# Optimization experiments

Hardware: AMD Instinct MI355X
Metric: run time of the kernel (lower is better)

Reference implementation:

```python
import jax, jax.numpy as jnp
import numpy as np

N_NODES = 100000
HIDDEN = 128
N_EDGES = 640000


def setup_inputs() -> dict:
    key = jax.random.key(0)
    ks = jax.random.split(key, 7)
    x = jax.random.normal(ks[0], (N_NODES, HIDDEN), dtype=jnp.float32)
    # torch Linear weights, stored transposed for y = h @ W + b
    W1 = jax.random.normal(ks[1], (HIDDEN, HIDDEN), dtype=jnp.float32) * (1.0 / np.sqrt(HIDDEN))
    b1 = jax.random.normal(ks[2], (HIDDEN,), dtype=jnp.float32) * 0.01
    W2 = jax.random.normal(ks[3], (HIDDEN, 1), dtype=jnp.float32) * (1.0 / np.sqrt(HIDDEN))
    b2 = jax.random.normal(ks[4], (1,), dtype=jnp.float32) * 0.01
    edge_index = jax.random.randint(ks[5], (2, N_EDGES), 0, N_NODES, dtype=jnp.int64 if jax.config.jax_enable_x64 else jnp.int32)
    edge_index_neg = jax.random.randint(ks[6], (2, N_EDGES), 0, N_NODES, dtype=jnp.int64 if jax.config.jax_enable_x64 else jnp.int32)
    return {"x": x, "W1": W1, "b1": b1, "W2": W2, "b2": b2,
            "edge_index": edge_index, "edge_index_neg": edge_index_neg}


def _decode(x, W1, b1, W2, b2, ei):
    # gather endpoints and Hadamard product: [E, hidden]
    h = x[ei[0]] * x[ei[1]]
    # decoder = ReLU -> Linear(h,h) -> ReLU -> Linear(h,1); then sigmoid
    h = jax.nn.relu(h)
    h = jax.nn.relu(h @ W1 + b1)
    return jax.nn.sigmoid(h @ W2 + b2)  # [E, 1]


def reference(x, W1, b1, W2, b2, edge_index, edge_index_neg):
    edge_pos_pred = _decode(x, W1, b1, W2, b2, edge_index)
    edge_neg_pred = _decode(x, W1, b1, W2, b2, edge_index_neg)
    return jnp.concatenate([edge_pos_pred, edge_neg_pred], axis=0)  # [2E, 1]
```

## Files before the change

### kernel.cpp

```cpp
#include <hip/hip_runtime.h>
#include <hip/hip_bf16.h>

#define HID   128
#define PITCH 136
#define TPB   256

typedef __attribute__((ext_vector_type(8))) __bf16 bf16x8;
typedef __attribute__((ext_vector_type(4))) __bf16 bf16x4;
typedef __attribute__((ext_vector_type(4))) float  f32x4;

__global__ __launch_bounds__(TPB) void prep_kernel(
    const float* __restrict__ W1, __bf16* __restrict__ w1t,
    const float* __restrict__ x, __bf16* __restrict__ xb, int n_x4) {
  if (xb) {
    for (int i = blockIdx.x * TPB + threadIdx.x; i < n_x4; i += gridDim.x * TPB) {
      float4 a = reinterpret_cast<const float4*>(x)[i];
      bf16x4 v;
      v[0] = (__bf16)a.x; v[1] = (__bf16)a.y; v[2] = (__bf16)a.z; v[3] = (__bf16)a.w;
      reinterpret_cast<bf16x4*>(xb)[i] = v;
    }
  }
  if (blockIdx.x == 0 && w1t) {
    __shared__ float w[HID * HID];
    for (int i = threadIdx.x; i < HID * HID; i += TPB) w[i] = W1[i];
    __syncthreads();
    for (int c = threadIdx.x; c < HID * (HID / 8); c += TPB) {
      int n  = c >> 4;
      int k0 = (c & 15) << 3;
      bf16x8 v;
#pragma unroll
      for (int j = 0; j < 8; ++j) v[j] = (__bf16)w[(k0 + j) * HID + n];
      *reinterpret_cast<bf16x8*>(&w1t[n * PITCH + k0]) = v;
    }
  }
}

__global__ __launch_bounds__(TPB) void vgae_decode_kernel(
    const __bf16* __restrict__ xb,
    const __bf16* __restrict__ w1t,
    const float* __restrict__ b1,
    const float* __restrict__ W2,
    const float* __restrict__ b2,
    const int* __restrict__ eip,
    const int* __restrict__ ein,
    float* __restrict__ out,
    int E, int n_tiles)
{
  __shared__ __bf16 sW[HID * PITCH];
  __shared__ float  sb1[HID];
  __shared__ float  sw2[HID];

  {
    const uint4* srcp = reinterpret_cast<const uint4*>(w1t);
    uint4*       dstp = reinterpret_cast<uint4*>(sW);
    for (int i = threadIdx.x; i < (HID * PITCH) / 8; i += TPB) dstp[i] = srcp[i];
  }
  if (threadIdx.x < HID) {
    sb1[threadIdx.x] = b1[threadIdx.x];
    sw2[threadIdx.x] = W2[threadIdx.x];
  }
  __syncthreads();

  const int lane = threadIdx.x & 63;
  const int wave = threadIdx.x >> 6;
  const int m    = lane & 15;
  const int quad = lane >> 4;
  const float b2v = b2[0];

  int tile = blockIdx.x;
  int nsrc = 0, ndst = 0;
  if (tile < n_tiles) {
    const int e_base = tile * 64 + wave * 16;
    const int* ei = (e_base < E) ? eip : ein;
    const int  eo = (e_base < E) ? e_base : (e_base - E);
    nsrc = ei[eo + m];
    ndst = ei[E + eo + m];
  }

  for (; tile < n_tiles; tile += gridDim.x) {
    const int src = nsrc, dst = ndst;
    const __bf16* xs = xb + (size_t)src * HID;
    const __bf16* xd = xb + (size_t)dst * HID;

    bf16x8 S[4], D[4];
#pragma unroll
    for (int kt = 0; kt < 4; ++kt) {
      const int k0 = kt * 32 + quad * 8;
      S[kt] = *reinterpret_cast<const bf16x8*>(xs + k0);
      D[kt] = *reinterpret_cast<const bf16x8*>(xd + k0);
    }

    const int tn = tile + gridDim.x;
    if (tn < n_tiles) {
      const int e_base = tn * 64 + wave * 16;
      const int* ei = (e_base < E) ? eip : ein;
      const int  eo = (e_base < E) ? e_base : (e_base - E);
      nsrc = ei[eo + m];
      ndst = ei[E + eo + m];
    }

    f32x4 acc[8] = {};

#pragma unroll
    for (int kt = 0; kt < 4; ++kt) {
      const int k0 = kt * 32 + quad * 8;
      bf16x8 a;
#pragma unroll
      for (int j = 0; j < 8; ++j) {
        float p = (float)S[kt][j] * (float)D[kt][j];
        a[j] = (__bf16)fmaxf(p, 0.f);
      }
#pragma unroll
      for (int nt = 0; nt < 8; ++nt) {
        bf16x8 bfr = *reinterpret_cast<const bf16x8*>(&sW[(nt * 16 + m) * PITCH + k0]);
        acc[nt] = __builtin_amdgcn_mfma_f32_16x16x32_bf16(a, bfr, acc[nt], 0, 0, 0);
      }
    }

    float p[4] = {0.f, 0.f, 0.f, 0.f};
#pragma unroll
    for (int nt = 0; nt < 8; ++nt) {
      const int n = nt * 16 + m;
      const float b1n = sb1[n];
      const float w2n = sw2[n];
#pragma unroll
      for (int r = 0; r < 4; ++r) {
        float t = fmaxf(acc[nt][r] + b1n, 0.f);
        p[r] = fmaf(t, w2n, p[r]);
      }
    }
#pragma unroll
    for (int off = 1; off < 16; off <<= 1) {
#pragma unroll
      for (int r = 0; r < 4; ++r) p[r] += __shfl_xor(p[r], off, 64);
    }
    if (m == 0) {
      float4 o;
      o.x = 1.f / (1.f + __expf(-(p[0] + b2v)));
      o.y = 1.f / (1.f + __expf(-(p[1] + b2v)));
      o.z = 1.f / (1.f + __expf(-(p[2] + b2v)));
      o.w = 1.f / (1.f + __expf(-(p[3] + b2v)));
      *reinterpret_cast<float4*>(out + tile * 64 + wave * 16 + quad * 4) = o;
    }
  }
}

__global__ __launch_bounds__(TPB) void vgae_decode_fallback(
    const float* __restrict__ x,
    const float* __restrict__ W1,
    const float* __restrict__ b1,
    const float* __restrict__ W2,
    const float* __restrict__ b2,
    const int* __restrict__ eip,
    const int* __restrict__ ein,
    float* __restrict__ out,
    int E, int n_tiles)
{
  __shared__ __bf16 sW[HID * PITCH];
  __shared__ float  sb1[HID];
  __shared__ float  sw2[HID];
  for (int c = threadIdx.x; c < HID * (HID / 8); c += TPB) {
    int n = c >> 4, k0 = (c & 15) << 3;
    bf16x8 v;
#pragma unroll
    for (int j = 0; j < 8; ++j) v[j] = (__bf16)W1[(k0 + j) * HID + n];
    *reinterpret_cast<bf16x8*>(&sW[n * PITCH + k0]) = v;
  }
  if (threadIdx.x < HID) { sb1[threadIdx.x] = b1[threadIdx.x]; sw2[threadIdx.x] = W2[threadIdx.x]; }
  __syncthreads();
  const int lane = threadIdx.x & 63, wave = threadIdx.x >> 6;
  const int m = lane & 15, quad = lane >> 4;
  const float b2v = b2[0];
  for (int tile = blockIdx.x; tile < n_tiles; tile += gridDim.x) {
    const int e_base = tile * 64 + wave * 16;
    const int* ei = (e_base < E) ? eip : ein;
    const int  eo = (e_base < E) ? e_base : (e_base - E);
    const int src = ei[eo + m], dst = ei[E + eo + m];
    const float* xs = x + (size_t)src * HID;
    const float* xd = x + (size_t)dst * HID;
    f32x4 acc[8] = {};
#pragma unroll
    for (int kt = 0; kt < 4; ++kt) {
      const int k0 = kt * 32 + quad * 8;
      float4 s0 = *reinterpret_cast<const float4*>(xs + k0);
      float4 s1 = *reinterpret_cast<const float4*>(xs + k0 + 4);
      float4 d0 = *reinterpret_cast<const float4*>(xd + k0);
      float4 d1 = *reinterpret_cast<const float4*>(xd + k0 + 4);
      bf16x8 a;
      a[0] = (__bf16)fmaxf(s0.x * d0.x, 0.f); a[1] = (__bf16)fmaxf(s0.y * d0.y, 0.f);
      a[2] = (__bf16)fmaxf(s0.z * d0.z, 0.f); a[3] = (__bf16)fmaxf(s0.w * d0.w, 0.f);
      a[4] = (__bf16)fmaxf(s1.x * d1.x, 0.f); a[5] = (__bf16)fmaxf(s1.y * d1.y, 0.f);
      a[6] = (__bf16)fmaxf(s1.z * d1.z, 0.f); a[7] = (__bf16)fmaxf(s1.w * d1.w, 0.f);
#pragma unroll
      for (int nt = 0; nt < 8; ++nt) {
        bf16x8 bfr = *reinterpret_cast<const bf16x8*>(&sW[(nt * 16 + m) * PITCH + k0]);
        acc[nt] = __builtin_amdgcn_mfma_f32_16x16x32_bf16(a, bfr, acc[nt], 0, 0, 0);
      }
    }
    float p[4] = {0.f, 0.f, 0.f, 0.f};
#pragma unroll
    for (int nt = 0; nt < 8; ++nt) {
      const int n = nt * 16 + m;
      const float b1n = sb1[n], w2n = sw2[n];
#pragma unroll
      for (int r = 0; r < 4; ++r) p[r] = fmaf(fmaxf(acc[nt][r] + b1n, 0.f), w2n, p[r]);
    }
#pragma unroll
    for (int off = 1; off < 16; off <<= 1)
#pragma unroll
      for (int r = 0; r < 4; ++r) p[r] += __shfl_xor(p[r], off, 64);
    if (m == 0) {
      float4 o;
      o.x = 1.f / (1.f + __expf(-(p[0] + b2v)));
      o.y = 1.f / (1.f + __expf(-(p[1] + b2v)));
      o.z = 1.f / (1.f + __expf(-(p[2] + b2v)));
      o.w = 1.f / (1.f + __expf(-(p[3] + b2v)));
      *reinterpret_cast<float4*>(out + tile * 64 + wave * 16 + quad * 4) = o;
    }
  }
}

extern "C" void kernel_launch(void* const* d_in, const int* in_sizes, int n_in,
                              void* d_out, int out_size, void* d_ws, size_t ws_size,
                              hipStream_t stream) {
  const float* x  = (const float*)d_in[0];
  const float* W1 = (const float*)d_in[1];
  const float* b1 = (const float*)d_in[2];
  const float* W2 = (const float*)d_in[3];
  const float* b2 = (const float*)d_in[4];
  const int*  eip = (const int*)d_in[5];
  const int*  ein = (const int*)d_in[6];
  float* out = (float*)d_out;
  const int E = in_sizes[5] / 2;
  const int n_tiles = (2 * E) / 64;
  const int n_nodes = in_sizes[0] / HID;
  const int n_x4 = in_sizes[0] / 4;

  const size_t w1t_bytes = (size_t)HID * PITCH * sizeof(__bf16);
  const size_t xb_off    = 65536;
  const size_t xb_bytes  = (size_t)n_nodes * HID * sizeof(__bf16);

  __bf16* w1t = nullptr;
  __bf16* xb  = nullptr;
  if (ws_size >= w1t_bytes) w1t = (__bf16*)d_ws;
  if (ws_size >= xb_off + xb_bytes) xb = (__bf16*)((char*)d_ws + xb_off);

  if (w1t && xb) {
    int prep_grid = (n_x4 + TPB - 1) / TPB;
    if (prep_grid > 6400) prep_grid = 6400;
    prep_kernel<<<prep_grid, TPB, 0, stream>>>(W1, w1t, x, xb, n_x4);
    vgae_decode_kernel<<<2560, TPB, 0, stream>>>(xb, w1t, b1, W2, b2,
                                                 eip, ein, out, E, n_tiles);
  } else {
    vgae_decode_fallback<<<2560, TPB, 0, stream>>>(x, W1, b1, W2, b2,
                                                   eip, ein, out, E, n_tiles);
  }
}
```

Baseline: 225.3 us.

## Keep W1 fragments in registers and software-pipeline node row gathers

The decode kernel no longer stages W1 in shared memory. Each lane now loads its B-fragments for all 8x4 MFMA tiles, plus b1 and W2, into registers once. The gathered source and destination rows for the next tile are prefetched while the current tile's MFMAs run, and node indices are fetched two tiles ahead. The bias is folded into the accumulator init, and the prep kernel transposes W1 across all blocks instead of through a single block's LDS. The grid shrinks to 1024 blocks with launch_bounds(256,2). In exchange, register pressure rises sharply (128 VGPRs for weights alone), which can limit occupancy or cause spills.

Result: slower. 243.7 us (+8.2%).

```diff
diff --git a/kernel.cpp b/kernel.cpp
--- a/kernel.cpp
+++ b/kernel.cpp
@@ -20,22 +20,20 @@
       reinterpret_cast<bf16x4*>(xb)[i] = v;
     }
   }
-  if (blockIdx.x == 0 && w1t) {
-    __shared__ float w[HID * HID];
-    for (int i = threadIdx.x; i < HID * HID; i += TPB) w[i] = W1[i];
-    __syncthreads();
-    for (int c = threadIdx.x; c < HID * (HID / 8); c += TPB) {
-      int n  = c >> 4;
-      int k0 = (c & 15) << 3;
+  if (w1t) {
+    const int gid = blockIdx.x * TPB + threadIdx.x;
+    if (gid < HID * (HID / 8)) {
+      const int n  = gid >> 4;
+      const int k0 = (gid & 15) << 3;
       bf16x8 v;
 #pragma unroll
-      for (int j = 0; j < 8; ++j) v[j] = (__bf16)w[(k0 + j) * HID + n];
-      *reinterpret_cast<bf16x8*>(&w1t[n * PITCH + k0]) = v;
-    }
-  }
-}
-
-__global__ __launch_bounds__(TPB) void vgae_decode_kernel(
+      for (int j = 0; j < 8; ++j) v[j] = (__bf16)W1[(k0 + j) * HID + n];
+      *reinterpret_cast<bf16x8*>(&w1t[n * HID + k0]) = v;
+    }
+  }
+}
+
+__global__ __launch_bounds__(TPB, 2) void vgae_decode_kernel(
     const __bf16* __restrict__ xb,
     const __bf16* __restrict__ w1t,
     const float* __restrict__ b1,
@@ -46,50 +44,49 @@
     float* __restrict__ out,
     int E, int n_tiles)
 {
-  __shared__ __bf16 sW[HID * PITCH];
-  __shared__ float  sb1[HID];
-  __shared__ float  sw2[HID];
-
-  {
-    const uint4* srcp = reinterpret_cast<const uint4*>(w1t);
-    uint4*       dstp = reinterpret_cast<uint4*>(sW);
-    for (int i = threadIdx.x; i < (HID * PITCH) / 8; i += TPB) dstp[i] = srcp[i];
-  }
-  if (threadIdx.x < HID) {
-    sb1[threadIdx.x] = b1[threadIdx.x];
-    sw2[threadIdx.x] = W2[threadIdx.x];
-  }
-  __syncthreads();
-
   const int lane = threadIdx.x & 63;
   const int wave = threadIdx.x >> 6;
   const int m    = lane & 15;
   const int quad = lane >> 4;
   const float b2v = b2[0];
 
+  bf16x8 Bf[8][4];
+#pragma unroll
+  for (int nt = 0; nt < 8; ++nt)
+#pragma unroll
+    for (int kt = 0; kt < 4; ++kt)
+      Bf[nt][kt] = *reinterpret_cast<const bf16x8*>(
+          w1t + (nt * 16 + m) * HID + kt * 32 + quad * 8);
+
+  float b1v[8], w2v[8];
+#pragma unroll
+  for (int nt = 0; nt < 8; ++nt) {
+    b1v[nt] = b1[nt * 16 + m];
+    w2v[nt] = W2[nt * 16 + m];
+  }
+
   int tile = blockIdx.x;
+  if (tile >= n_tiles) return;
+
+  bf16x8 S[4], D[4];
   int nsrc = 0, ndst = 0;
-  if (tile < n_tiles) {
+
+  {
     const int e_base = tile * 64 + wave * 16;
     const int* ei = (e_base < E) ? eip : ein;
     const int  eo = (e_base < E) ? e_base : (e_base - E);
-    nsrc = ei[eo + m];
-    ndst = ei[E + eo + m];
-  }
-
-  for (; tile < n_tiles; tile += gridDim.x) {
-    const int src = nsrc, dst = ndst;
-    const __bf16* xs = xb + (size_t)src * HID;
-    const __bf16* xd = xb + (size_t)dst * HID;
-
-    bf16x8 S[4], D[4];
+    const int s0 = ei[eo + m];
+    const int d0 = ei[E + eo + m];
+    const __bf16* xs = xb + (size_t)s0 * HID;
+    const __bf16* xd = xb + (size_t)d0 * HID;
 #pragma unroll
     for (int kt = 0; kt < 4; ++kt) {
       const int k0 = kt * 32 + quad * 8;
       S[kt] = *reinterpret_cast<const bf16x8*>(xs + k0);
       D[kt] = *reinterpret_cast<const bf16x8*>(xd + k0);
     }
-
+  }
+  {
     const int tn = tile + gridDim.x;
     if (tn < n_tiles) {
       const int e_base = tn * 64 + wave * 16;
@@ -98,8 +95,29 @@
       nsrc = ei[eo + m];
       ndst = ei[E + eo + m];
     }
-
-    f32x4 acc[8] = {};
+  }
+
+  for (; tile < n_tiles; tile += gridDim.x) {
+    const int tn = tile + gridDim.x;
+    const __bf16* nxs = xb + (size_t)nsrc * HID;
+    const __bf16* nxd = xb + (size_t)ndst * HID;
+
+    const int tnn = tn + gridDim.x;
+    if (tnn < n_tiles) {
+      const int e_base = tnn * 64 + wave * 16;
+      const int* ei = (e_base < E) ? eip : ein;
+      const int  eo = (e_base < E) ? e_base : (e_base - E);
+      nsrc = ei[eo + m];
+      ndst = ei[E + eo + m];
+    }
+
+    f32x4 acc[8];
+#pragma unroll
+    for (int nt = 0; nt < 8; ++nt) {
+      f32x4 t;
+      t[0] = b1v[nt]; t[1] = b1v[nt]; t[2] = b1v[nt]; t[3] = b1v[nt];
+      acc[nt] = t;
+    }
 
 #pragma unroll
     for (int kt = 0; kt < 4; ++kt) {
@@ -107,27 +125,24 @@
       bf16x8 a;
 #pragma unroll
       for (int j = 0; j < 8; ++j) {
-        float p = (float)S[kt][j] * (float)D[kt][j];
-        a[j] = (__bf16)fmaxf(p, 0.f);
+        float pr = (float)S[kt][j] * (float)D[kt][j];
+        a[j] = (__bf16)fmaxf(pr, 0.f);
       }
-#pragma unroll
-      for (int nt = 0; nt < 8; ++nt) {
-        bf16x8 bfr = *reinterpret_cast<const bf16x8*>(&sW[(nt * 16 + m) * PITCH + k0]);
-        acc[nt] = __builtin_amdgcn_mfma_f32_16x16x32_bf16(a, bfr, acc[nt], 0, 0, 0);
+      if (tn < n_tiles) {
+        S[kt] = *reinterpret_cast<const bf16x8*>(nxs + k0);
+        D[kt] = *reinterpret_cast<const bf16x8*>(nxd + k0);
       }
+#pragma unroll
+      for (int nt = 0; nt < 8; ++nt)
+        acc[nt] = __builtin_amdgcn_mfma_f32_16x16x32_bf16(a, Bf[nt][kt], acc[nt], 0, 0, 0);
     }
 
     float p[4] = {0.f, 0.f, 0.f, 0.f};
 #pragma unroll
     for (int nt = 0; nt < 8; ++nt) {
-      const int n = nt * 16 + m;
-      const float b1n = sb1[n];
-      const float w2n = sw2[n];
-#pragma unroll
-      for (int r = 0; r < 4; ++r) {
-        float t = fmaxf(acc[nt][r] + b1n, 0.f);
-        p[r] = fmaf(t, w2n, p[r]);
-      }
+#pragma unroll
+      for (int r = 0; r < 4; ++r)
+        p[r] = fmaf(fmaxf(acc[nt][r], 0.f), w2v[nt], p[r]);
     }
 #pragma unroll
     for (int off = 1; off < 16; off <<= 1) {
@@ -236,7 +251,7 @@
   const int n_nodes = in_sizes[0] / HID;
   const int n_x4 = in_sizes[0] / 4;
 
-  const size_t w1t_bytes = (size_t)HID * PITCH * sizeof(__bf16);
+  const size_t w1t_bytes = (size_t)HID * HID * sizeof(__bf16);
   const size_t xb_off    = 65536;
   const size_t xb_bytes  = (size_t)n_nodes * HID * sizeof(__bf16);
 
@@ -249,7 +264,7 @@
     int prep_grid = (n_x4 + TPB - 1) / TPB;
     if (prep_grid > 6400) prep_grid = 6400;
     prep_kernel<<<prep_grid, TPB, 0, stream>>>(W1, w1t, x, xb, n_x4);
-    vgae_decode_kernel<<<2560, TPB, 0, stream>>>(xb, w1t, b1, W2, b2,
+    vgae_decode_kernel<<<1024, TPB, 0, stream>>>(xb, w1t, b1, W2, b2,
                                                  eip, ein, out, E, n_tiles);
   } else {
     vgae_decode_fallback<<<2560, TPB, 0, stream>>>(x, W1, b1, W2, b2,
```
